# Optimization experiments

Hardware: AMD Instinct MI355X
Metric: run time of the kernel (lower is better)

The kernel has to match this reference:

```python
import jax, jax.numpy as jnp
import numpy as np

B, T, DE, DD, A, FN, FS = 32, 2000, 512, 1024, 128, 32, 16
TEMPERATURE = 1.0


def setup_inputs() -> dict:
    key = jax.random.key(0)
    ks = jax.random.split(key, 10)
    input_enc = jax.random.normal(ks[0], (B, T, DE), dtype=jnp.float32)
    # lengths in [T//2, T] so no zero-length utterances
    enc_lengths = jax.random.randint(ks[1], (B,), T // 2, T + 1, dtype=jnp.int32)
    input_dec = jax.random.normal(ks[2], (B, DD), dtype=jnp.float32)
    # prev_att: previous-step attention weights (masked, normalized)
    prev_att = jax.random.uniform(ks[3], (B, T), dtype=jnp.float32)
    pad = jnp.arange(T)[None, :] >= enc_lengths[:, None]
    prev_att = jnp.where(pad, 0.0, prev_att)
    prev_att = prev_att / jnp.sum(prev_att, axis=1, keepdims=True)
    # parameters
    conv_w = jax.random.normal(ks[4], (FN, 1, 2 * FS + 1), dtype=jnp.float32) * 0.1  # [out,in,k]
    enc_w = jax.random.normal(ks[5], (A, DE), dtype=jnp.float32) * 0.04
    dec_w = jax.random.normal(ks[6], (A, DD), dtype=jnp.float32) * 0.03
    att_w = jax.random.normal(ks[7], (A, FN), dtype=jnp.float32) * 0.17
    att_b = jnp.zeros((A,), dtype=jnp.float32)
    out_w = jax.random.normal(ks[8], (1, A), dtype=jnp.float32) * 0.09
    return dict(input_enc=input_enc, enc_lengths=enc_lengths, input_dec=input_dec,
                prev_att=prev_att, conv_w=conv_w, enc_w=enc_w, dec_w=dec_w,
                att_w=att_w, att_b=att_b, out_w=out_w)


def reference(input_enc, enc_lengths, input_dec, prev_att,
              conv_w, enc_w, dec_w, att_w, att_b, out_w):
    b, t, _ = input_enc.shape
    fs = (conv_w.shape[-1] - 1) // 2  # 'same' padding
    # padding mask: True at padded positions t >= length
    mask = jnp.arange(t)[None, :] >= enc_lengths[:, None]  # [B,T]
    # location features: Conv1d over prev attention, 1 -> FN channels, same length
    conv = jax.lax.conv_general_dilated(
        prev_att[:, None, :], conv_w, window_strides=(1,),
        padding=[(fs, fs)], dimension_numbers=("NCH", "OIH", "NCH"))  # [B,FN,T]
    loc_feat = conv.transpose(0, 2, 1)  # [B,T,FN]
    projected_att = loc_feat @ att_w.T + att_b        # [B,T,A]
    projected_enc = input_enc @ enc_w.T               # [B,T,A]
    projected_dec = (input_dec @ dec_w.T)[:, None, :]  # [B,1,A]
    score = jnp.squeeze(jnp.tanh(projected_att + projected_enc + projected_dec) @ out_w.T, -1)  # [B,T]
    score = jnp.where(mask, -jnp.inf, score)
    att_weight = jax.nn.softmax(TEMPERATURE * score, axis=1)  # [B,T]
    context = jnp.einsum("btd,bt->bd", input_enc, att_weight)  # [B,DE]
    return context, att_weight
```

## Files before the change

### kernel.cpp

```cpp
#include <hip/hip_runtime.h>
#include <hip/hip_bf16.h>
#include <math.h>

#define B_ 32
#define T_ 2000
#define DE_ 512
#define DD_ 1024
#define A_ 128
#define FN_ 32
#define FS_ 16
#define KW_ (2*FS_+1)

typedef __bf16 bf16x8 __attribute__((ext_vector_type(8)));
typedef __bf16 bf16x4 __attribute__((ext_vector_type(4)));
typedef float f32x4 __attribute__((ext_vector_type(4)));

#define BT 256
#define LSTR 40

__device__ __forceinline__ void load_lds16(const void* g, void* l) {
    __builtin_amdgcn_global_load_lds(
        (const __attribute__((address_space(1))) unsigned int*)g,
        (__attribute__((address_space(3))) unsigned int*)l, 16, 0, 0);
}

__device__ __forceinline__ bf16x8 cvt8(float4 x, float4 y) {
    bf16x8 o;
    o[0] = (__bf16)x.x; o[1] = (__bf16)x.y; o[2] = (__bf16)x.z; o[3] = (__bf16)x.w;
    o[4] = (__bf16)y.x; o[5] = (__bf16)y.y; o[6] = (__bf16)y.z; o[7] = (__bf16)y.w;
    return o;
}

__global__ __launch_bounds__(256) void prep_kernel(
    const float* __restrict__ enc_w, const float* __restrict__ att_w,
    const float* __restrict__ input_dec, const float* __restrict__ dec_w,
    const float* __restrict__ att_b,
    __bf16* __restrict__ enc_bf, __bf16* __restrict__ att_bf,
    float* __restrict__ pdec, float* __restrict__ ctx_un )
{
    int bx = blockIdx.x, tid = threadIdx.x;
    if (bx < 64) {
        int i = bx * 256 + tid;
        float4 v = ((const float4*)enc_w)[i];
        bf16x4 o;
        o[0] = (__bf16)v.x; o[1] = (__bf16)v.y; o[2] = (__bf16)v.z; o[3] = (__bf16)v.w;
        *(bf16x4*)(enc_bf + (size_t)i * 4) = o;
        if (i < (A_ * FN_) / 4) {
            float4 w = ((const float4*)att_w)[i];
            bf16x4 p;
            p[0] = (__bf16)w.x; p[1] = (__bf16)w.y; p[2] = (__bf16)w.z; p[3] = (__bf16)w.w;
            *(bf16x4*)(att_bf + (size_t)i * 4) = p;
        }
    } else if (bx < 192) {
        int pb = bx - 64;
        int b  = pb >> 2;
        int a0 = (pb & 3) * 32;
        int al = tid >> 3;
        int kg = tid & 7;
        int a  = a0 + al;
        const float4* w = (const float4*)(dec_w + (size_t)a * DD_);
        const float4* x = (const float4*)(input_dec + (size_t)b * DD_);
        float acc = 0.f;
        #pragma unroll 8
        for (int j = 0; j < 32; j++) {
            int i4 = kg + j * 8;
            float4 wv = w[i4], xv = x[i4];
            acc += wv.x * xv.x + wv.y * xv.y + wv.z * xv.z + wv.w * xv.w;
        }
        acc += __shfl_xor(acc, 1, 64);
        acc += __shfl_xor(acc, 2, 64);
        acc += __shfl_xor(acc, 4, 64);
        if (kg == 0) pdec[b * A_ + a] = acc + att_b[a];
    } else {
        int idx = (bx - 192) * 256 + tid;
        if (idx < (B_ * DE_ + B_) / 4 + 1)
            ((float4*)ctx_un)[idx] = make_float4(0.f, 0.f, 0.f, 0.f);
    }
}

__global__ __launch_bounds__(1024, 4) void score_kernel(
    const float* __restrict__ input_enc, const __bf16* __restrict__ enc_bf,
    const float* __restrict__ prev_att,  const float* __restrict__ conv_w,
    const __bf16* __restrict__ att_bf,   const float* __restrict__ pdec,
    const float* __restrict__ out_w,     const int* __restrict__ lengths,
    float* __restrict__ wbuf, float* __restrict__ ctx_un,
    float* __restrict__ denom)
{
    __shared__ __align__(16) char Bt[8][16384];
    __shared__ __align__(16) float pa_s[BT + 2 * FS_];
    __shared__ __align__(16) __bf16 loc_s[BT * LSTR];
    __shared__ float w_s[BT];

    const int tid  = threadIdx.x;
    const int lane = tid & 63;
    const int wv   = tid >> 6;
    const int b  = blockIdx.y;
    const int t0 = blockIdx.x * BT;
    const int len = lengths[b];

    #pragma unroll
    for (int j = 0; j < 8; j++) {
        int w  = wv * 64 + lane;
        int r  = w >> 3;
        int cp = w & 7;
        int c  = cp ^ (r & 7);
        load_lds16(enc_bf + (size_t)r * DE_ + j * 64 + c * 8,
                   Bt[j] + wv * 1024);
    }

    const int f    = tid & 31;
    const int rblk = tid >> 5;
    float cwr[KW_];
    #pragma unroll
    for (int k = 0; k < KW_; k++) cwr[k] = conv_w[f * KW_ + k];

    if (tid < BT + 2 * FS_) {
        int t = t0 - FS_ + tid;
        pa_s[tid] = (t >= 0 && t < T_) ? prev_att[b * T_ + t] : 0.f;
    }
    __syncthreads();

    {
        float par[40];
        #pragma unroll
        for (int j = 0; j < 10; j++)
            *(float4*)&par[j * 4] = *(const float4*)&pa_s[rblk * 8 + j * 4];
        float accv[8] = {0.f, 0.f, 0.f, 0.f, 0.f, 0.f, 0.f, 0.f};
        #pragma unroll
        for (int k = 0; k < KW_; k++) {
            float c = cwr[k];
            #pragma unroll
            for (int j = 0; j < 8; j++) accv[j] += par[j + k] * c;
        }
        #pragma unroll
        for (int j = 0; j < 8; j++)
            loc_s[(rblk * 8 + j) * LSTR + f] = (__bf16)accv[j];
    }
    __syncthreads();

    const int col  = lane & 15;
    const int grp  = lane >> 4;
    const int rowb = wv * 16 + col;
    const int t_row = t0 + rowb;
    const int t_clamp = t_row < T_ ? t_row : T_ - 1;
    const int sw = (col & 7);

    f32x4 acc[8];
    const f32x4 zero = (f32x4){0.f, 0.f, 0.f, 0.f};

    {
        bf16x8 afrag = *(const bf16x8*)(loc_s + rowb * LSTR + grp * 8);
        #pragma unroll
        for (int i = 0; i < 8; i++) {
            bf16x8 bfrag = *(const bf16x8*)(att_bf + (size_t)(i * 16 + col) * FN_ + grp * 8);
            acc[i] = __builtin_amdgcn_mfma_f32_16x16x32_bf16(afrag, bfrag, zero, 0, 0, 0);
        }
    }

    const float* arow = input_enc + ((size_t)(b * T_ + t_clamp)) * DE_ + grp * 8;

    #pragma unroll
    for (int it = 0; it < 8; ++it) {
        const int kc = it * 64;
        float4 r0 = *(const float4*)(arow + kc);
        float4 r1 = *(const float4*)(arow + kc + 4);
        float4 r2 = *(const float4*)(arow + kc + 32);
        float4 r3 = *(const float4*)(arow + kc + 36);
        bf16x8 af0 = cvt8(r0, r1);
        bf16x8 af1 = cvt8(r2, r3);

        #pragma unroll
        for (int i = 0; i < 8; i++) {
            bf16x8 bfrag = *(const bf16x8*)(Bt[it] + (i * 16 + col) * 128 + ((grp ^ sw) * 16));
            acc[i] = __builtin_amdgcn_mfma_f32_16x16x32_bf16(af0, bfrag, acc[i], 0, 0, 0);
        }
        #pragma unroll
        for (int i = 0; i < 8; i++) {
            bf16x8 bfrag = *(const bf16x8*)(Bt[it] + (i * 16 + col) * 128 + (((4 + grp) ^ sw) * 16));
            acc[i] = __builtin_amdgcn_mfma_f32_16x16x32_bf16(af1, bfrag, acc[i], 0, 0, 0);
        }
    }

    float s[4] = {0.f, 0.f, 0.f, 0.f};
    float Mabs = 0.f;
    #pragma unroll
    for (int i = 0; i < 8; i++) {
        int a = i * 16 + col;
        float ow = out_w[a];
        Mabs += fabsf(ow);
        float bias = pdec[b * A_ + a];
        #pragma unroll
        for (int r = 0; r < 4; r++) {
            float v = acc[i][r] + bias;
            v = fminf(fmaxf(v, -15.f), 15.f);
            float e = __expf(2.f * v);
            s[r] += ow * ((e - 1.f) / (e + 1.f));
        }
    }
    #pragma unroll
    for (int r = 0; r < 4; r++) {
        s[r] += __shfl_xor(s[r], 1, 64);
        s[r] += __shfl_xor(s[r], 2, 64);
        s[r] += __shfl_xor(s[r], 4, 64);
        s[r] += __shfl_xor(s[r], 8, 64);
    }
    Mabs += __shfl_xor(Mabs, 1, 64);
    Mabs += __shfl_xor(Mabs, 2, 64);
    Mabs += __shfl_xor(Mabs, 4, 64);
    Mabs += __shfl_xor(Mabs, 8, 64);

    if (col == 0) {
        #pragma unroll
        for (int r = 0; r < 4; r++) {
            int rl = wv * 16 + grp * 4 + r;
            int t = t0 + rl;
            float w = 0.f;
            if (t < len) w = __expf(s[r] - Mabs);
            w_s[rl] = w;
            if (t < T_) wbuf[b * T_ + t] = w;
        }
    }
    __syncthreads();

    if (tid < 64) {
        float w = w_s[tid] + w_s[tid + 64] + w_s[tid + 128] + w_s[tid + 192];
        w += __shfl_xor(w, 1, 64);
        w += __shfl_xor(w, 2, 64);
        w += __shfl_xor(w, 4, 64);
        w += __shfl_xor(w, 8, 64);
        w += __shfl_xor(w, 16, 64);
        w += __shfl_xor(w, 32, 64);
        if (tid == 0) atomicAdd(&denom[b], w);
    }

    int n_eff = len - t0;
    if (n_eff > BT) n_eff = BT;
    if (n_eff > 0) {
        int rg  = tid >> 8;
        int d0  = (tid & 255) * 2;
        int rlo = rg * 64;
        int rhi = rlo + 64 < n_eff ? rlo + 64 : n_eff;
        if (rhi > rlo) {
            const float* ebase = input_enc + ((size_t)(b * T_ + t0 + rlo)) * DE_ + d0;
            float cx = 0.f, cy = 0.f;
            #pragma unroll 8
            for (int r = 0; r < rhi - rlo; r++) {
                float w = w_s[rlo + r];
                float2 v = *(const float2*)(ebase + (size_t)r * DE_);
                cx += w * v.x;
                cy += w * v.y;
            }
            atomicAdd(&ctx_un[b * DE_ + d0 + 0], cx);
            atomicAdd(&ctx_un[b * DE_ + d0 + 1], cy);
        }
    }
}

__global__ __launch_bounds__(256) void finalize_kernel(
    const float* __restrict__ wbuf, const float* __restrict__ ctx_un,
    const float* __restrict__ denom, float* __restrict__ out)
{
    int bx = blockIdx.x, tid = threadIdx.x;
    if (bx < 64) {
        int i4 = bx * 256 + tid;
        if (i4 < (B_ * T_) / 4) {
            int b = i4 / (T_ / 4);
            float inv = 1.f / denom[b];
            float4 w = ((const float4*)wbuf)[i4];
            w.x *= inv; w.y *= inv; w.z *= inv; w.w *= inv;
            ((float4*)(out + B_ * DE_))[i4] = w;
        }
    } else {
        int j = (bx - 64) * 256 + tid;
        int b = j / (DE_ / 4);
        float inv = 1.f / denom[b];
        float4 c = ((const float4*)ctx_un)[j];
        c.x *= inv; c.y *= inv; c.z *= inv; c.w *= inv;
        ((float4*)out)[j] = c;
    }
}

extern "C" void kernel_launch(void* const* d_in, const int* in_sizes, int n_in,
                              void* d_out, int out_size, void* d_ws, size_t ws_size,
                              hipStream_t stream)
{
    const float* input_enc   = (const float*)d_in[0];
    const int*   enc_lengths = (const int*)d_in[1];
    const float* input_dec   = (const float*)d_in[2];
    const float* prev_att    = (const float*)d_in[3];
    const float* conv_w      = (const float*)d_in[4];
    const float* enc_w       = (const float*)d_in[5];
    const float* dec_w       = (const float*)d_in[6];
    const float* att_w       = (const float*)d_in[7];
    const float* att_b       = (const float*)d_in[8];
    const float* out_w       = (const float*)d_in[9];

    float* out = (float*)d_out;
    char* ws = (char*)d_ws;
    float*  pdec   = (float*)ws;
    float*  wbuf   = (float*)(ws + 16384);
    __bf16* enc_bf = (__bf16*)(ws + 272384);
    __bf16* att_bf = (__bf16*)(ws + 403456);
    float*  ctx_un = (float*)(ws + 411648);
    float*  denom  = (float*)(ws + 477184);

    prep_kernel<<<209, 256, 0, stream>>>(enc_w, att_w, input_dec, dec_w, att_b,
                                         enc_bf, att_bf, pdec, ctx_un);

    dim3 sgrid((T_ + BT - 1) / BT, B_);
    score_kernel<<<sgrid, 1024, 0, stream>>>(input_enc, enc_bf, prev_att, conv_w,
                                             att_bf, pdec, out_w, enc_lengths,
                                             wbuf, ctx_un, denom);

    finalize_kernel<<<80, 256, 0, stream>>>(wbuf, ctx_un, denom, out);
}
```

Measured before the change: 240.6 us.

## Shrink score tile to 64 rows and double-buffer A/B chunks in LDS

The time tile drops from 256 to 64 rows with 256-thread blocks, giving four times as many workgroups. Encoder rows and the bf16 weight chunks are now streamed through two LDS buffers with async global-to-LDS loads, explicit vmcnt waits and barriers, replacing direct global loads of A and a fully preloaded weight matrix. The goal is to overlap memory traffic with MFMA work and raise occupancy. In exchange, every block reloads the whole enc_w, and there are more atomics on denom and ctx_un.

Measured after the change: 224.9 us. -6.5%, faster.

```diff
diff --git a/kernel.cpp b/kernel.cpp
--- a/kernel.cpp
+++ b/kernel.cpp
@@ -15,7 +15,7 @@
 typedef __bf16 bf16x4 __attribute__((ext_vector_type(4)));
 typedef float f32x4 __attribute__((ext_vector_type(4)));
 
-#define BT 256
+#define BT 64
 #define LSTR 40
 
 __device__ __forceinline__ void load_lds16(const void* g, void* l) {
@@ -24,10 +24,10 @@
         (__attribute__((address_space(3))) unsigned int*)l, 16, 0, 0);
 }
 
-__device__ __forceinline__ bf16x8 cvt8(float4 x, float4 y) {
+__device__ __forceinline__ bf16x8 cvt8v(f32x4 x, f32x4 y) {
     bf16x8 o;
-    o[0] = (__bf16)x.x; o[1] = (__bf16)x.y; o[2] = (__bf16)x.z; o[3] = (__bf16)x.w;
-    o[4] = (__bf16)y.x; o[5] = (__bf16)y.y; o[6] = (__bf16)y.z; o[7] = (__bf16)y.w;
+    o[0] = (__bf16)x[0]; o[1] = (__bf16)x[1]; o[2] = (__bf16)x[2]; o[3] = (__bf16)x[3];
+    o[4] = (__bf16)y[0]; o[5] = (__bf16)y[1]; o[6] = (__bf16)y[2]; o[7] = (__bf16)y[3];
     return o;
 }
 
@@ -78,7 +78,7 @@
     }
 }
 
-__global__ __launch_bounds__(1024, 4) void score_kernel(
+__global__ __launch_bounds__(256, 2) void score_kernel(
     const float* __restrict__ input_enc, const __bf16* __restrict__ enc_bf,
     const float* __restrict__ prev_att,  const float* __restrict__ conv_w,
     const __bf16* __restrict__ att_bf,   const float* __restrict__ pdec,
@@ -86,7 +86,8 @@
     float* __restrict__ wbuf, float* __restrict__ ctx_un,
     float* __restrict__ denom)
 {
-    __shared__ __align__(16) char Bt[8][16384];
+    __shared__ __align__(16) char At[2][16384];
+    __shared__ __align__(16) char Bt[2][16384];
     __shared__ __align__(16) float pa_s[BT + 2 * FS_];
     __shared__ __align__(16) __bf16 loc_s[BT * LSTR];
     __shared__ float w_s[BT];
@@ -98,15 +99,32 @@
     const int t0 = blockIdx.x * BT;
     const int len = lengths[b];
 
-    #pragma unroll
-    for (int j = 0; j < 8; j++) {
-        int w  = wv * 64 + lane;
-        int r  = w >> 3;
-        int cp = w & 7;
-        int c  = cp ^ (r & 7);
-        load_lds16(enc_bf + (size_t)r * DE_ + j * 64 + c * 8,
-                   Bt[j] + wv * 1024);
-    }
+    auto issueA = [&](int kc, int bufi) {
+        #pragma unroll
+        for (int j = 0; j < 4; j++) {
+            int s  = j * 256 + tid;
+            int r  = s >> 4;
+            int q  = s & 15;
+            int cl = q ^ (r & 15);
+            int t  = t0 + r; if (t > T_ - 1) t = T_ - 1;
+            load_lds16(input_enc + ((size_t)(b * T_ + t)) * DE_ + kc + cl * 4,
+                       At[bufi] + j * 4096 + wv * 1024);
+        }
+    };
+    auto issueB = [&](int kc, int bufi) {
+        #pragma unroll
+        for (int j = 0; j < 4; j++) {
+            int s  = j * 256 + tid;
+            int r  = s >> 3;
+            int cp = s & 7;
+            int c  = cp ^ (r & 7);
+            load_lds16(enc_bf + (size_t)r * DE_ + kc + c * 8,
+                       Bt[bufi] + j * 4096 + wv * 1024);
+        }
+    };
+
+    issueA(0, 0);  issueB(0, 0);
+    issueA(64, 1); issueB(64, 1);
 
     const int f    = tid & 31;
     const int rblk = tid >> 5;
@@ -141,9 +159,8 @@
     const int col  = lane & 15;
     const int grp  = lane >> 4;
     const int rowb = wv * 16 + col;
-    const int t_row = t0 + rowb;
-    const int t_clamp = t_row < T_ ? t_row : T_ - 1;
-    const int sw = (col & 7);
+    const int sw   = (col & 7);
+    const int key  = rowb & 15;
 
     f32x4 acc[8];
     const f32x4 zero = (f32x4){0.f, 0.f, 0.f, 0.f};
@@ -157,28 +174,39 @@
         }
     }
 
-    const float* arow = input_enc + ((size_t)(b * T_ + t_clamp)) * DE_ + grp * 8;
+    auto compute = [&](const char* Ab, const char* Bb) {
+        f32x4 v0 = *(const f32x4*)(Ab + rowb * 256 + ((grp * 2)     ^ key) * 16);
+        f32x4 v1 = *(const f32x4*)(Ab + rowb * 256 + ((grp * 2 + 1) ^ key) * 16);
+        f32x4 v2 = *(const f32x4*)(Ab + rowb * 256 + ((8 + grp * 2)     ^ key) * 16);
+        f32x4 v3 = *(const f32x4*)(Ab + rowb * 256 + ((8 + grp * 2 + 1) ^ key) * 16);
+        bf16x8 af0 = cvt8v(v0, v1);
+        bf16x8 af1 = cvt8v(v2, v3);
+        #pragma unroll
+        for (int i = 0; i < 8; i++) {
+            bf16x8 bfrag = *(const bf16x8*)(Bb + (i * 16 + col) * 128 + ((grp ^ sw) * 16));
+            acc[i] = __builtin_amdgcn_mfma_f32_16x16x32_bf16(af0, bfrag, acc[i], 0, 0, 0);
+        }
+        #pragma unroll
+        for (int i = 0; i < 8; i++) {
+            bf16x8 bfrag = *(const bf16x8*)(Bb + (i * 16 + col) * 128 + (((4 + grp) ^ sw) * 16));
+            acc[i] = __builtin_amdgcn_mfma_f32_16x16x32_bf16(af1, bfrag, acc[i], 0, 0, 0);
+        }
+    };
 
     #pragma unroll
     for (int it = 0; it < 8; ++it) {
-        const int kc = it * 64;
-        float4 r0 = *(const float4*)(arow + kc);
-        float4 r1 = *(const float4*)(arow + kc + 4);
-        float4 r2 = *(const float4*)(arow + kc + 32);
-        float4 r3 = *(const float4*)(arow + kc + 36);
-        bf16x8 af0 = cvt8(r0, r1);
-        bf16x8 af1 = cvt8(r2, r3);
-
-        #pragma unroll
-        for (int i = 0; i < 8; i++) {
-            bf16x8 bfrag = *(const bf16x8*)(Bt[it] + (i * 16 + col) * 128 + ((grp ^ sw) * 16));
-            acc[i] = __builtin_amdgcn_mfma_f32_16x16x32_bf16(af0, bfrag, acc[i], 0, 0, 0);
-        }
-        #pragma unroll
-        for (int i = 0; i < 8; i++) {
-            bf16x8 bfrag = *(const bf16x8*)(Bt[it] + (i * 16 + col) * 128 + (((4 + grp) ^ sw) * 16));
-            acc[i] = __builtin_amdgcn_mfma_f32_16x16x32_bf16(af1, bfrag, acc[i], 0, 0, 0);
-        }
+        compute(At[it & 1], Bt[it & 1]);
+        if (it == 7) break;
+        __builtin_amdgcn_s_barrier();
+        if (it + 2 < 8) {
+            issueA((it + 2) * 64, it & 1);
+            issueB((it + 2) * 64, it & 1);
+            asm volatile("s_waitcnt vmcnt(8)" ::: "memory");
+        } else {
+            asm volatile("s_waitcnt vmcnt(0)" ::: "memory");
+        }
+        __builtin_amdgcn_s_barrier();
+        __builtin_amdgcn_sched_barrier(0);
     }
 
     float s[4] = {0.f, 0.f, 0.f, 0.f};
@@ -223,7 +251,7 @@
     __syncthreads();
 
     if (tid < 64) {
-        float w = w_s[tid] + w_s[tid + 64] + w_s[tid + 128] + w_s[tid + 192];
+        float w = w_s[tid];
         w += __shfl_xor(w, 1, 64);
         w += __shfl_xor(w, 2, 64);
         w += __shfl_xor(w, 4, 64);
@@ -236,23 +264,18 @@
     int n_eff = len - t0;
     if (n_eff > BT) n_eff = BT;
     if (n_eff > 0) {
-        int rg  = tid >> 8;
-        int d0  = (tid & 255) * 2;
-        int rlo = rg * 64;
-        int rhi = rlo + 64 < n_eff ? rlo + 64 : n_eff;
-        if (rhi > rlo) {
-            const float* ebase = input_enc + ((size_t)(b * T_ + t0 + rlo)) * DE_ + d0;
-            float cx = 0.f, cy = 0.f;
-            #pragma unroll 8
-            for (int r = 0; r < rhi - rlo; r++) {
-                float w = w_s[rlo + r];
-                float2 v = *(const float2*)(ebase + (size_t)r * DE_);
-                cx += w * v.x;
-                cy += w * v.y;
-            }
-            atomicAdd(&ctx_un[b * DE_ + d0 + 0], cx);
-            atomicAdd(&ctx_un[b * DE_ + d0 + 1], cy);
-        }
+        int d0 = tid * 2;
+        const float* ebase = input_enc + ((size_t)(b * T_ + t0)) * DE_ + d0;
+        float cx = 0.f, cy = 0.f;
+        #pragma unroll 8
+        for (int t = 0; t < n_eff; t++) {
+            float w = w_s[t];
+            float2 v = *(const float2*)(ebase + (size_t)t * DE_);
+            cx += w * v.x;
+            cy += w * v.y;
+        }
+        atomicAdd(&ctx_un[b * DE_ + d0 + 0], cx);
+        atomicAdd(&ctx_un[b * DE_ + d0 + 1], cy);
     }
 }
 
@@ -308,9 +331,9 @@
                                          enc_bf, att_bf, pdec, ctx_un);
 
     dim3 sgrid((T_ + BT - 1) / BT, B_);
-    score_kernel<<<sgrid, 1024, 0, stream>>>(input_enc, enc_bf, prev_att, conv_w,
-                                             att_bf, pdec, out_w, enc_lengths,
-                                             wbuf, ctx_un, denom);
+    score_kernel<<<sgrid, 256, 0, stream>>>(input_enc, enc_bf, prev_att, conv_w,
+                                            att_bf, pdec, out_w, enc_lengths,
+                                            wbuf, ctx_un, denom);
 
     finalize_kernel<<<80, 256, 0, stream>>>(wbuf, ctx_un, denom, out);
 }
```

## Software-pipeline encoder loads, halve tile size, skip fully padded tiles

Applied to the files above, without the earlier changes.

Halves the time tile to 128 rows with 512-thread blocks. Encoder rows are prefetched four K-steps ahead through inline-asm global loads and explicit vmcnt waits, so the loads overlap the MFMA work. Blocks whose tile lies entirely past the sequence length now only zero their weights and exit early. The context reduction is simplified to one column per thread, and the grid doubles, so the LDS copy of the weight matrix is duplicated across more blocks.

Result: faster. 229.7 us (-4.5%).

```diff
diff --git a/kernel.cpp b/kernel.cpp
--- a/kernel.cpp
+++ b/kernel.cpp
@@ -15,7 +15,7 @@
 typedef __bf16 bf16x4 __attribute__((ext_vector_type(4)));
 typedef float f32x4 __attribute__((ext_vector_type(4)));
 
-#define BT 256
+#define BT 128
 #define LSTR 40
 
 __device__ __forceinline__ void load_lds16(const void* g, void* l) {
@@ -24,10 +24,16 @@
         (__attribute__((address_space(3))) unsigned int*)l, 16, 0, 0);
 }
 
-__device__ __forceinline__ bf16x8 cvt8(float4 x, float4 y) {
+__device__ __forceinline__ f32x4 gload4(const float* p) {
+    f32x4 d;
+    asm volatile("global_load_dwordx4 %0, %1, off" : "=v"(d) : "v"(p));
+    return d;
+}
+
+__device__ __forceinline__ bf16x8 cvt8v(f32x4 x, f32x4 y) {
     bf16x8 o;
-    o[0] = (__bf16)x.x; o[1] = (__bf16)x.y; o[2] = (__bf16)x.z; o[3] = (__bf16)x.w;
-    o[4] = (__bf16)y.x; o[5] = (__bf16)y.y; o[6] = (__bf16)y.z; o[7] = (__bf16)y.w;
+    o[0] = (__bf16)x[0]; o[1] = (__bf16)x[1]; o[2] = (__bf16)x[2]; o[3] = (__bf16)x[3];
+    o[4] = (__bf16)y[0]; o[5] = (__bf16)y[1]; o[6] = (__bf16)y[2]; o[7] = (__bf16)y[3];
     return o;
 }
 
@@ -78,7 +84,7 @@
     }
 }
 
-__global__ __launch_bounds__(1024, 4) void score_kernel(
+__global__ __launch_bounds__(512, 1) void score_kernel(
     const float* __restrict__ input_enc, const __bf16* __restrict__ enc_bf,
     const float* __restrict__ prev_att,  const float* __restrict__ conv_w,
     const __bf16* __restrict__ att_bf,   const float* __restrict__ pdec,
@@ -86,7 +92,7 @@
     float* __restrict__ wbuf, float* __restrict__ ctx_un,
     float* __restrict__ denom)
 {
-    __shared__ __align__(16) char Bt[8][16384];
+    __shared__ __align__(16) char BtAll[8][16384];
     __shared__ __align__(16) float pa_s[BT + 2 * FS_];
     __shared__ __align__(16) __bf16 loc_s[BT * LSTR];
     __shared__ float w_s[BT];
@@ -98,45 +104,13 @@
     const int t0 = blockIdx.x * BT;
     const int len = lengths[b];
 
-    #pragma unroll
-    for (int j = 0; j < 8; j++) {
-        int w  = wv * 64 + lane;
-        int r  = w >> 3;
-        int cp = w & 7;
-        int c  = cp ^ (r & 7);
-        load_lds16(enc_bf + (size_t)r * DE_ + j * 64 + c * 8,
-                   Bt[j] + wv * 1024);
-    }
-
-    const int f    = tid & 31;
-    const int rblk = tid >> 5;
-    float cwr[KW_];
-    #pragma unroll
-    for (int k = 0; k < KW_; k++) cwr[k] = conv_w[f * KW_ + k];
-
-    if (tid < BT + 2 * FS_) {
-        int t = t0 - FS_ + tid;
-        pa_s[tid] = (t >= 0 && t < T_) ? prev_att[b * T_ + t] : 0.f;
-    }
-    __syncthreads();
-
-    {
-        float par[40];
-        #pragma unroll
-        for (int j = 0; j < 10; j++)
-            *(float4*)&par[j * 4] = *(const float4*)&pa_s[rblk * 8 + j * 4];
-        float accv[8] = {0.f, 0.f, 0.f, 0.f, 0.f, 0.f, 0.f, 0.f};
-        #pragma unroll
-        for (int k = 0; k < KW_; k++) {
-            float c = cwr[k];
-            #pragma unroll
-            for (int j = 0; j < 8; j++) accv[j] += par[j + k] * c;
-        }
-        #pragma unroll
-        for (int j = 0; j < 8; j++)
-            loc_s[(rblk * 8 + j) * LSTR + f] = (__bf16)accv[j];
-    }
-    __syncthreads();
+    if (t0 >= len) {
+        if (tid < BT) {
+            int t = t0 + tid;
+            if (t < T_) wbuf[b * T_ + t] = 0.f;
+        }
+        return;
+    }
 
     const int col  = lane & 15;
     const int grp  = lane >> 4;
@@ -145,6 +119,58 @@
     const int t_clamp = t_row < T_ ? t_row : T_ - 1;
     const int sw = (col & 7);
 
+    const float* arow = input_enc + ((size_t)(b * T_ + t_clamp)) * DE_ + grp * 8;
+
+    f32x4 pipe[4][2];
+    #pragma unroll
+    for (int c2 = 0; c2 < 4; c2++) {
+        pipe[c2][0] = gload4(arow + c2 * 32);
+        pipe[c2][1] = gload4(arow + c2 * 32 + 4);
+    }
+
+    #pragma unroll
+    for (int j = 0; j < 8; j++) {
+        #pragma unroll
+        for (int jj = 0; jj < 2; jj++) {
+            int s  = jj * 512 + tid;
+            int r  = s >> 3;
+            int cp = s & 7;
+            int c  = cp ^ (r & 7);
+            load_lds16(enc_bf + (size_t)r * DE_ + j * 64 + c * 8,
+                       (char*)BtAll + j * 16384 + jj * 8192 + wv * 1024);
+        }
+    }
+
+    const int f    = tid & 31;
+    const int rblk = tid >> 5;
+    float cwr[KW_];
+    #pragma unroll
+    for (int k = 0; k < KW_; k++) cwr[k] = conv_w[f * KW_ + k];
+
+    if (tid < BT + 2 * FS_) {
+        int t = t0 - FS_ + tid;
+        pa_s[tid] = (t >= 0 && t < T_) ? prev_att[b * T_ + t] : 0.f;
+    }
+    __syncthreads();
+
+    {
+        float par[40];
+        #pragma unroll
+        for (int j = 0; j < 10; j++)
+            *(float4*)&par[j * 4] = *(const float4*)&pa_s[rblk * 8 + j * 4];
+        float accv[8] = {0.f, 0.f, 0.f, 0.f, 0.f, 0.f, 0.f, 0.f};
+        #pragma unroll
+        for (int k = 0; k < KW_; k++) {
+            float c = cwr[k];
+            #pragma unroll
+            for (int j = 0; j < 8; j++) accv[j] += par[j + k] * c;
+        }
+        #pragma unroll
+        for (int j = 0; j < 8; j++)
+            loc_s[(rblk * 8 + j) * LSTR + f] = (__bf16)accv[j];
+    }
+    __syncthreads();
+
     f32x4 acc[8];
     const f32x4 zero = (f32x4){0.f, 0.f, 0.f, 0.f};
 
@@ -157,29 +183,27 @@
         }
     }
 
-    const float* arow = input_enc + ((size_t)(b * T_ + t_clamp)) * DE_ + grp * 8;
-
-    #pragma unroll
-    for (int it = 0; it < 8; ++it) {
-        const int kc = it * 64;
-        float4 r0 = *(const float4*)(arow + kc);
-        float4 r1 = *(const float4*)(arow + kc + 4);
-        float4 r2 = *(const float4*)(arow + kc + 32);
-        float4 r3 = *(const float4*)(arow + kc + 36);
-        bf16x8 af0 = cvt8(r0, r1);
-        bf16x8 af1 = cvt8(r2, r3);
-
-        #pragma unroll
-        for (int i = 0; i < 8; i++) {
-            bf16x8 bfrag = *(const bf16x8*)(Bt[it] + (i * 16 + col) * 128 + ((grp ^ sw) * 16));
-            acc[i] = __builtin_amdgcn_mfma_f32_16x16x32_bf16(af0, bfrag, acc[i], 0, 0, 0);
-        }
-        #pragma unroll
-        for (int i = 0; i < 8; i++) {
-            bf16x8 bfrag = *(const bf16x8*)(Bt[it] + (i * 16 + col) * 128 + (((4 + grp) ^ sw) * 16));
-            acc[i] = __builtin_amdgcn_mfma_f32_16x16x32_bf16(af1, bfrag, acc[i], 0, 0, 0);
-        }
-    }
+#define KSTEP(IT, CNT) { \
+    asm volatile("s_waitcnt vmcnt(" #CNT ")" \
+                 : "+v"(pipe[(IT) % 4][0]), "+v"(pipe[(IT) % 4][1])); \
+    bf16x8 af = cvt8v(pipe[(IT) % 4][0], pipe[(IT) % 4][1]); \
+    const char* Bb = (const char*)BtAll + ((IT) >> 1) * 16384; \
+    _Pragma("unroll") \
+    for (int i = 0; i < 8; i++) { \
+        bf16x8 bfrag = *(const bf16x8*)(Bb + (i * 16 + col) * 128 + \
+                                        ((((IT) & 1) * 4 + grp) ^ sw) * 16); \
+        acc[i] = __builtin_amdgcn_mfma_f32_16x16x32_bf16(af, bfrag, acc[i], 0, 0, 0); \
+    } \
+    if ((IT) + 4 <= 15) { \
+        pipe[(IT) % 4][0] = gload4(arow + ((IT) + 4) * 32); \
+        pipe[(IT) % 4][1] = gload4(arow + ((IT) + 4) * 32 + 4); \
+    } \
+}
+    KSTEP(0, 6)  KSTEP(1, 6)  KSTEP(2, 6)  KSTEP(3, 6)
+    KSTEP(4, 6)  KSTEP(5, 6)  KSTEP(6, 6)  KSTEP(7, 6)
+    KSTEP(8, 6)  KSTEP(9, 6)  KSTEP(10, 6) KSTEP(11, 6)
+    KSTEP(12, 6) KSTEP(13, 4) KSTEP(14, 2) KSTEP(15, 0)
+#undef KSTEP
 
     float s[4] = {0.f, 0.f, 0.f, 0.f};
     float Mabs = 0.f;
@@ -223,7 +247,7 @@
     __syncthreads();
 
     if (tid < 64) {
-        float w = w_s[tid] + w_s[tid + 64] + w_s[tid + 128] + w_s[tid + 192];
+        float w = w_s[tid] + w_s[tid + 64];
         w += __shfl_xor(w, 1, 64);
         w += __shfl_xor(w, 2, 64);
         w += __shfl_xor(w, 4, 64);
@@ -236,23 +260,13 @@
     int n_eff = len - t0;
     if (n_eff > BT) n_eff = BT;
     if (n_eff > 0) {
-        int rg  = tid >> 8;
-        int d0  = (tid & 255) * 2;
-        int rlo = rg * 64;
-        int rhi = rlo + 64 < n_eff ? rlo + 64 : n_eff;
-        if (rhi > rlo) {
-            const float* ebase = input_enc + ((size_t)(b * T_ + t0 + rlo)) * DE_ + d0;
-            float cx = 0.f, cy = 0.f;
-            #pragma unroll 8
-            for (int r = 0; r < rhi - rlo; r++) {
-                float w = w_s[rlo + r];
-                float2 v = *(const float2*)(ebase + (size_t)r * DE_);
-                cx += w * v.x;
-                cy += w * v.y;
-            }
-            atomicAdd(&ctx_un[b * DE_ + d0 + 0], cx);
-            atomicAdd(&ctx_un[b * DE_ + d0 + 1], cy);
-        }
+        int d0 = tid;
+        const float* ebase = input_enc + ((size_t)(b * T_ + t0)) * DE_ + d0;
+        float cx = 0.f;
+        #pragma unroll 8
+        for (int t = 0; t < n_eff; t++)
+            cx += w_s[t] * ebase[(size_t)t * DE_];
+        atomicAdd(&ctx_un[b * DE_ + d0], cx);
     }
 }
 
@@ -308,9 +322,9 @@
                                          enc_bf, att_bf, pdec, ctx_un);
 
     dim3 sgrid((T_ + BT - 1) / BT, B_);
-    score_kernel<<<sgrid, 1024, 0, stream>>>(input_enc, enc_bf, prev_att, conv_w,
-                                             att_bf, pdec, out_w, enc_lengths,
-                                             wbuf, ctx_un, denom);
+    score_kernel<<<sgrid, 512, 0, stream>>>(input_enc, enc_bf, prev_att, conv_w,
+                                            att_bf, pdec, out_w, enc_lengths,
+                                            wbuf, ctx_un, denom);
 
     finalize_kernel<<<80, 256, 0, stream>>>(wbuf, ctx_un, denom, out);
 }
```
